# Kernel optimization log

Measured on AMD Instinct MI355X. Metric: run time of the kernel, lower is better.

Reference implementation:

```python
import jax, jax.numpy as jnp
import numpy as np

B, N, X_DIM, Y_DIM, H_DIM, R_DIM = 64, 512, 128, 128, 4096, 1024


def setup_inputs() -> dict:
    key = jax.random.key(0)
    ks = jax.random.split(key, 10)
    x = jax.random.normal(ks[0], (B, N, X_DIM), dtype=jnp.float32)
    y = jax.random.normal(ks[1], (B, N, Y_DIM), dtype=jnp.float32)
    # per-sample context lengths in [1, N]; prefix mask guarantees >=1 True per row
    lengths = jax.random.randint(ks[2], (B,), 1, N + 1)
    mask = (jnp.arange(N)[None, :] < lengths[:, None])  # [B, N] bool
    d_in = X_DIM + Y_DIM
    s1 = 1.0 / np.sqrt(d_in)
    s2 = 1.0 / np.sqrt(H_DIM)
    W1 = jax.random.uniform(ks[3], (d_in, H_DIM), jnp.float32, -s1, s1)
    b1 = jax.random.uniform(ks[4], (H_DIM,), jnp.float32, -s1, s1)
    W2 = jax.random.uniform(ks[5], (H_DIM, H_DIM), jnp.float32, -s2, s2)
    b2 = jax.random.uniform(ks[6], (H_DIM,), jnp.float32, -s2, s2)
    W3 = jax.random.uniform(ks[7], (H_DIM, R_DIM), jnp.float32, -s2, s2)
    b3 = jax.random.uniform(ks[8], (R_DIM,), jnp.float32, -s2, s2)
    return {"x": x, "y": y, "mask": mask,
            "W1": W1, "b1": b1, "W2": W2, "b2": b2, "W3": W3, "b3": b3}


def reference(x, y, mask, W1, b1, W2, b2, W3, b3):
    # Dense equivalent of gather -> MLP -> scatter_mean by batch id:
    # the MLP is pointwise over tokens, so applying it densely and taking a
    # masked mean over the point dim gives identical math to the ragged path.
    nn_in = jnp.concatenate([x, y], axis=-1)          # [B, N, x+y]
    h = jax.nn.relu(jnp.einsum('bnd,dh->bnh', nn_in, W1) + b1)
    h = jax.nn.relu(jnp.einsum('bnh,hk->bnk', h, W2) + b2)
    r = jnp.einsum('bnk,kr->bnr', h, W3) + b3          # [B, N, r_dim]
    m = mask.astype(r.dtype)[..., None]                # [B, N, 1]
    counts = jnp.maximum(m.sum(axis=1), 1.0)           # [B, 1]
    r_aggr = (r * m).sum(axis=1) / counts              # [B, r_dim]
    return r_aggr
```

## Files before the change

### kernel.cpp

```cpp
#include <hip/hip_runtime.h>


using u16 = unsigned short;
using u8 = unsigned char;
typedef float f32x4 __attribute__((ext_vector_type(4)));
typedef short s16x8 __attribute__((ext_vector_type(8)));
typedef int i32x4 __attribute__((ext_vector_type(4)));

__device__ __forceinline__ u16 f2bf(float f) {
  union { float f; unsigned u; } v; v.f = f;
  unsigned r = (v.u + 0x7fffu + ((v.u >> 16) & 1u)) >> 16;
  return (u16)r;
}


__global__ void count_k(const int* __restrict__ mask, int* __restrict__ lens) {
  int b = blockIdx.x, l = threadIdx.x;
  const int4* row = (const int4*)(mask + (size_t)b * 512);
  int4 v0 = row[l];
  int4 v1 = row[l + 64];
  int s = v0.x + v0.y + v0.z + v0.w + v1.x + v1.y + v1.z + v1.w;
  #pragma unroll
  for (int o = 32; o; o >>= 1) s += __shfl_down(s, o);
  if (l == 0) lens[b] = s;
}

__global__ void meta_k(const int* __restrict__ lens, int* __restrict__ meta) {
  if (threadIdx.x == 0) {
    int acc = 0; meta[0] = 0;
    for (int b = 0; b < 64; ++b) { acc += lens[b]; meta[b + 1] = acc; }
    meta[65] = acc;
    meta[66] = (acc + 127) >> 7;
  }
}

__global__ void tok2b_k(const int* __restrict__ meta, int* __restrict__ tok2b) {
  int i = blockIdx.x * 256 + threadIdx.x;
  int total = meta[65];
  int b = 64;
  if (i < total) {
    int lo = 0, hi = 64;
    while (hi - lo > 1) { int mid = (lo + hi) >> 1; if (meta[mid] <= i) lo = mid; else hi = mid; }
    b = lo;
  }
  tok2b[i] = b;
}

__global__ void build_a(const float* __restrict__ x, const float* __restrict__ y,
                        const int* __restrict__ meta, const int* __restrict__ tok2b,
                        u16* __restrict__ A) {
  int i4 = blockIdx.x * 256 + threadIdx.x;
  int e = i4 * 4;
  int m = e >> 8, c = e & 255;
  int total = meta[65];
  ushort4 o = {0, 0, 0, 0};
  if (m < total) {
    int b = tok2b[m], t = m - meta[b];
    const float* src = (c < 128) ? x + ((size_t)b * 512 + t) * 128 + c
                                 : y + ((size_t)b * 512 + t) * 128 + (c - 128);
    float4 v = *(const float4*)src;
    o.x = f2bf(v.x); o.y = f2bf(v.y); o.z = f2bf(v.z); o.w = f2bf(v.w);
  }
  *(ushort4*)&A[e] = o;
}

__global__ void pack_k(const float* __restrict__ W, u16* __restrict__ P,
                       int N, int NKB) {
  long c = (long)blockIdx.x * 256 + threadIdx.x;
  int lane = c & 63; long r = c >> 6;
  int s = r & 1; int j = (r >> 1) & 3; int wn = (r >> 3) & 1;
  long q = r >> 4;
  int ktb = (int)(q % NKB), nt = (int)(q / NKB);
  int k = ktb * 64 + s * 32 + (lane >> 4) * 8;
  int n = nt * 128 + wn * 64 + j * 16 + (lane & 15);
  ushort o[8];
  #pragma unroll
  for (int e = 0; e < 8; ++e) o[e] = f2bf(W[(size_t)(k + e) * N + n]);
  *(uint4*)&P[c * 8] = *(uint4*)o;
}

__global__ void colmax_k(const float* __restrict__ W, float* __restrict__ cmax) {
  int n = blockIdx.x * 256 + threadIdx.x;
  int k0 = blockIdx.y * 128;
  float m = 0.f;
  for (int k = k0; k < k0 + 128; ++k)
    m = fmaxf(m, fabsf(W[(size_t)k * 4096 + n]));
  atomicMax((int*)&cmax[n], __float_as_int(m));
}

__global__ void pack8_k(const float* __restrict__ W, const float* __restrict__ cmax,
                        char* __restrict__ P) {
  long c = (long)blockIdx.x * 256 + threadIdx.x;
  int lane = c & 63; long r = c >> 6;
  int j = r & 3; int wn = (r >> 2) & 1; long q = r >> 3;
  int ktb = (int)(q & 63), nt = (int)(q >> 6);
  int k = ktb * 64 + (lane >> 4) * 16;
  int n = nt * 128 + wn * 64 + j * 16 + (lane & 15);
  float rw = 127.0f / fmaxf(cmax[n], 1e-20f);
  char o[16];
  #pragma unroll
  for (int e = 0; e < 16; ++e) {
    int v = __float2int_rn(W[(size_t)(k + e) * 4096 + n] * rw);
    v = v > 127 ? 127 : (v < -127 ? -127 : v);
    o[e] = (char)v;
  }
  *(uint4*)&P[c * 16] = *(const uint4*)o;
}

__global__ void sn_k(const float* __restrict__ S, const int* __restrict__ lens,
                     u16* __restrict__ Sn) {
  int i4 = blockIdx.x * 256 + threadIdx.x;
  int e = i4 * 4;
  int m = e >> 12;
  float inv = (m < 64) ? (1.0f / (float)lens[m]) : 0.0f;
  float4 v = *(const float4*)(S + e);
  ushort4 o;
  o.x = f2bf(v.x * inv); o.y = f2bf(v.y * inv);
  o.z = f2bf(v.z * inv); o.w = f2bf(v.w * inv);
  *(ushort4*)&Sn[e] = o;
}

template <int MODE>
__global__ __launch_bounds__(256, 3) void gemm_k(
    const void* __restrict__ Av, int lda, const void* __restrict__ BPv,
    const float* __restrict__ bias, const float* __restrict__ cmax,
    u8* __restrict__ Hout, float* __restrict__ Sout, float* __restrict__ Fout,
    const int* __restrict__ meta, const int* __restrict__ tok2b,
    int K, int Nld, int tile0, int tile_cap) {
  constexpr bool A8 = (MODE == 1);
  constexpr int BK = A8 ? 128 : 64;
  __shared__ union {
    u16 a16[2][128 * 64];
    u8  a8[3][128 * 128];
    u8  outT8[128 * 128];
  } sm;

  const int tid = threadIdx.x;
  const int wave = tid >> 6;
  const int lane = tid & 63;
  const int wm = wave >> 1, wn = wave & 1;
  const int quad = lane >> 4, l15 = lane & 15;
  const int NKB = K >> 6;

  int nslots;
  if constexpr (MODE < 2) {
    int tc = meta[66] - tile0;
    tc = tc < 0 ? 0 : (tc > tile_cap ? tile_cap : tc);
    nslots = tc * 32;
  } else {
    nslots = gridDim.x;
  }

  for (int slot = blockIdx.x; slot < nslots; slot += gridDim.x) {
    int mt, n0, k0, kend;
    if constexpr (MODE < 2) {
      mt = slot >> 5; n0 = (slot & 31) << 7; k0 = 0; kend = K;
    } else {
      mt = 0; n0 = slot << 7; k0 = blockIdx.y * 512; kend = k0 + 512;
    }

    f32x4 accf[4][4];
    i32x4 acci[4][4];
    #pragma unroll
    for (int i = 0; i < 4; i++)
      #pragma unroll
      for (int j = 0; j < 4; j++) {
        if constexpr (A8) acci[i][j] = (i32x4){0, 0, 0, 0};
        else accf[i][j] = (f32x4){0.f, 0.f, 0.f, 0.f};
      }

    const u8* ag8[4];
    const u16* ag16[4];
    if constexpr (A8) {
      #pragma unroll
      for (int il = 0; il < 4; ++il) {
        int ci = (wave * 4 + il) * 64 + lane;
        int m = ci >> 3, c = (ci & 7) ^ (m & 7);
        ag8[il] = (const u8*)Av + (size_t)(mt * 128 + m) * lda + c * 16;
      }
    } else {
      #pragma unroll
      for (int il = 0; il < 4; ++il) {
        int ci = (wave * 4 + il) * 64 + lane;
        int m = ci >> 3, c = (ci & 7) ^ (m & 7);
        ag16[il] = (const u16*)Av + (size_t)(mt * 128 + m) * lda + c * 8;
      }
    }
    const u16* bw = nullptr;
    const u8* bw8 = nullptr;
    if constexpr (A8)
      bw8 = (const u8*)BPv + (size_t)(n0 >> 7) * NKB * 8192 + wn * 4096 + lane * 16;
    else
      bw = (const u16*)BPv + (size_t)(n0 >> 7) * NKB * 8192 + wn * 4096 + lane * 8;

    s16x8 breg0[8], breg1[8];
    i32x4 breg8_0[8], breg8_1[8];

    auto stageA = [&](int kt, int buf) {
      if constexpr (A8) {
        #pragma unroll
        for (int il = 0; il < 4; ++il)
          __builtin_amdgcn_global_load_lds(
              (const __attribute__((address_space(1))) void*)(ag8[il] + kt),
              (__attribute__((address_space(3))) void*)(&sm.a8[buf][(wave * 4 + il) * 1024]),
              16, 0, 0);
      } else {
        #pragma unroll
        for (int il = 0; il < 4; ++il)
          __builtin_amdgcn_global_load_lds(
              (const __attribute__((address_space(1))) void*)(ag16[il] + kt),
              (__attribute__((address_space(3))) void*)(&sm.a16[buf][(wave * 4 + il) * 512]),
              16, 0, 0);
      }
    };
    auto loadB = [&](int kt, int which) {
      if constexpr (A8) {
        i32x4* dst = which ? breg8_1 : breg8_0;
        const u8* p = bw8 + (size_t)(kt >> 6) * 8192;
        #pragma unroll
        for (int s = 0; s < 2; s++)
          #pragma unroll
          for (int j = 0; j < 4; j++)
            dst[s * 4 + j] = *(const i32x4*)(p + s * 8192 + j * 1024);
      } else {
        s16x8* dst = which ? breg1 : breg0;
        const u16* p = bw + (size_t)(kt >> 6) * 8192;
        #pragma unroll
        for (int j = 0; j < 4; j++)
          #pragma unroll
          for (int s = 0; s < 2; s++)
            dst[j * 2 + s] = *(const s16x8*)(p + j * 1024 + s * 512);
      }
    };
    auto compute = [&](int buf, int which) {
      if constexpr (A8) {
        const i32x4* br = which ? breg8_1 : breg8_0;
        const u8* ab = &sm.a8[0][0] + buf * 16384;
        #pragma unroll
        for (int s = 0; s < 2; ++s) {
          #pragma unroll
          for (int i = 0; i < 4; i++) {
            int m = wm * 64 + i * 16 + l15;
            int c = (s * 4 + quad) ^ (m & 7);
            i32x4 a = *(const i32x4*)&ab[(m * 8 + c) * 16];
            #pragma unroll
            for (int j = 0; j < 4; j++)
              acci[i][j] = __builtin_amdgcn_mfma_i32_16x16x64_i8(
                  a, br[s * 4 + j], acci[i][j], 0, 0, 0);
          }
        }
      } else {
        const s16x8* br = which ? breg1 : breg0;
        #pragma unroll
        for (int s = 0; s < 2; ++s) {
          s16x8 af[4];
          #pragma unroll
          for (int i = 0; i < 4; i++) {
            int m = wm * 64 + i * 16 + l15;
            int c = (s * 4 + quad) ^ (m & 7);
            af[i] = *(const s16x8*)&sm.a16[buf][(m * 8 + c) * 8];
          }
          #pragma unroll
          for (int i = 0; i < 4; i++)
            #pragma unroll
            for (int j = 0; j < 4; j++)
              accf[i][j] = __builtin_amdgcn_mfma_f32_16x16x32_bf16(
                  af[i], br[j * 2 + s], accf[i][j], 0, 0, 0);
        }
      }
    };

    if constexpr (A8) {
      stageA(k0, 0);
      stageA(k0 + BK, 1);
      loadB(k0, 0);
      const int NP = (kend - k0) / BK;
      int bufc = 0, bufs = 2;
      for (int t = 0; t < NP; t += 2) {
        int kt = k0 + t * BK;
        __builtin_amdgcn_s_waitcnt(0x0F7C);
        __builtin_amdgcn_s_barrier();
        if (t + 2 < NP) stageA(kt + 2 * BK, bufs);
        __builtin_amdgcn_sched_barrier(0);
        loadB(kt + BK, 1);
        compute(bufc, 0);
        bufc = bufc == 2 ? 0 : bufc + 1;
        bufs = bufs == 2 ? 0 : bufs + 1;
        __builtin_amdgcn_s_waitcnt(0x0F7C);
        __builtin_amdgcn_s_barrier();
        if (t + 3 < NP) stageA(kt + 3 * BK, bufs);
        __builtin_amdgcn_sched_barrier(0);
        if (t + 2 < NP) loadB(kt + 2 * BK, 0);
        compute(bufc, 1);
        bufc = bufc == 2 ? 0 : bufc + 1;
        bufs = bufs == 2 ? 0 : bufs + 1;
      }
    } else {
      stageA(k0, 0);
      loadB(k0, 0);
      const int NP = (kend - k0) / BK;
      for (int t = 0; t < NP; t += 2) {
        int kt = k0 + t * BK;
        __builtin_amdgcn_s_waitcnt(0x0F78);
        __builtin_amdgcn_s_barrier();
        stageA(kt + BK, 1);
        __builtin_amdgcn_sched_barrier(0);
        loadB(kt + BK, 1);
        compute(0, 0);
        __builtin_amdgcn_s_waitcnt(0x0F78);
        __builtin_amdgcn_s_barrier();
        if (t + 2 < NP) {
          stageA(kt + 2 * BK, 0);
          __builtin_amdgcn_sched_barrier(0);
          loadB(kt + 2 * BK, 0);
        }
        compute(1, 1);
      }
    }
    __syncthreads();

    if constexpr (MODE == 0) {
      float bb[4];
      #pragma unroll
      for (int j = 0; j < 4; j++) bb[j] = bias[n0 + wn * 64 + j * 16 + l15];
      #pragma unroll
      for (int i = 0; i < 4; i++)
        #pragma unroll
        for (int j = 0; j < 4; j++) {
          int col = wn * 64 + j * 16 + l15;
          #pragma unroll
          for (int r = 0; r < 4; r++) {
            int row = wm * 64 + i * 16 + quad * 4 + r;
            float v = accf[i][j][r] + bb[j];
            v = v > 0.f ? v : 0.f;
            int qv = (int)(v * 32.0f + 0.5f);
            if (qv > 127) qv = 127;
            sm.outT8[row * 128 + col] = (u8)qv;
          }
        }
      __syncthreads();
      #pragma unroll
      for (int u = 0; u < 4; ++u) {
        int e = u * 256 + tid;
        int row = e >> 3, c16 = (e & 7) * 16;
        *(uint4*)&Hout[(size_t)(mt * 128 + row) * Nld + n0 + c16] =
            *(const uint4*)&sm.outT8[row * 128 + c16];
      }
      __syncthreads();
    } else if constexpr (MODE == 1) {
      float bb[4], sc[4];
      #pragma unroll
      for (int j = 0; j < 4; j++) {
        int col_ = n0 + wn * 64 + j * 16 + l15;
        bb[j] = bias[col_];
        sc[j] = cmax[col_] * (1.0f / (127.0f * 32.0f));
      }
      int tb[16];
      const int gbase = tile0 * 128 + mt * 128 + wm * 64 + quad * 4;
      #pragma unroll
      for (int i = 0; i < 4; i++)
        #pragma unroll
        for (int r = 0; r < 4; r++) tb[i * 4 + r] = tok2b[gbase + i * 16 + r];
      #pragma unroll
      for (int j = 0; j < 4; j++) {
        int col = n0 + wn * 64 + j * 16 + l15;
        float sum = 0.f;
        int cb = tb[0];
        #pragma unroll
        for (int idx = 0; idx < 16; ++idx) {
          float t = (float)acci[idx >> 2][j][idx & 3] * sc[j] + bb[j];
          t = t > 0.f ? t : 0.f;
          int b = tb[idx];
          if (b != cb) {
            atomicAdd(&Sout[(size_t)cb * 4096 + col], sum);
            sum = 0.f; cb = b;
          }
          sum += t;
        }
        atomicAdd(&Sout[(size_t)cb * 4096 + col], sum);
      }
    } else {
      float bb[4];
      #pragma unroll
      for (int j = 0; j < 4; j++)
        bb[j] = (blockIdx.y == 0) ? bias[n0 + wn * 64 + j * 16 + l15] : 0.f;
      #pragma unroll
      for (int i = 0; i < 4; i++)
        #pragma unroll
        for (int j = 0; j < 4; j++) {
          int col = wn * 64 + j * 16 + l15;
          #pragma unroll
          for (int r = 0; r < 4; r++) {
            int row = wm * 64 + i * 16 + quad * 4 + r;
            if (row < 64)
              atomicAdd(&Fout[(size_t)row * Nld + n0 + col], accf[i][j][r] + bb[j]);
          }
        }
    }
  }
}

extern "C" void kernel_launch(void* const* d_in, const int* in_sizes, int n_in,
                              void* d_out, int out_size, void* d_ws, size_t ws_size,
                              hipStream_t stream) {
  const float* x  = (const float*)d_in[0];
  const float* y  = (const float*)d_in[1];
  const int* mask = (const int*)d_in[2];
  const float* W1 = (const float*)d_in[3];
  const float* b1 = (const float*)d_in[4];
  const float* W2 = (const float*)d_in[5];
  const float* b2 = (const float*)d_in[6];
  const float* W3 = (const float*)d_in[7];
  const float* b3 = (const float*)d_in[8];
  float* out = (float*)d_out;

  char* ws = (char*)d_ws;
  size_t off = 0;
  auto alloc = [&](size_t bytes) {
    char* p = ws + off;
    off += (bytes + 255) & ~(size_t)255;
    return p;
  };
  int* lens  = (int*)alloc(64 * 4);
  int* meta  = (int*)alloc(70 * 4);
  int* tok2b = (int*)alloc((size_t)32768 * 4);
  float* S   = (float*)alloc((size_t)128 * 4096 * 4);
  u16* Sn    = (u16*)alloc((size_t)128 * 4096 * 2);
  float* cm  = (float*)alloc((size_t)4096 * 4);
  u16* W1P   = (u16*)alloc((size_t)256 * 4096 * 2);
  char* W2P8 = (char*)alloc((size_t)4096 * 4096);
  u16* W3P   = (u16*)alloc((size_t)4096 * 1024 * 2);
  u16* Abuf  = (u16*)alloc((size_t)32768 * 256 * 2);
  size_t fixed = off;
  size_t h1_full = (size_t)32768 * 4096;
  int nchunks, tile_cap;
  if (ws_size >= fixed + h1_full) { nchunks = 1; tile_cap = 256; }
  else if (ws_size >= fixed + h1_full / 2) { nchunks = 2; tile_cap = 128; }
  else if (ws_size >= fixed + h1_full / 4) { nchunks = 4; tile_cap = 64; }
  else return;
  u8* H1 = (u8*)alloc(h1_full / nchunks);

  hipMemsetAsync(S, 0, (size_t)128 * 4096 * 4, stream);
  hipMemsetAsync(cm, 0, (size_t)4096 * 4, stream);
  hipMemsetAsync(out, 0, (size_t)out_size * 4, stream);
  count_k<<<64, 64, 0, stream>>>(mask, lens);
  meta_k<<<1, 64, 0, stream>>>(lens, meta);
  tok2b_k<<<128, 256, 0, stream>>>(meta, tok2b);
  build_a<<<8192, 256, 0, stream>>>(x, y, meta, tok2b, Abuf);
  pack_k<<<512, 256, 0, stream>>>(W1, W1P, 4096, 4);
  colmax_k<<<dim3(16, 32), 256, 0, stream>>>(W2, cm);
  pack8_k<<<4096, 256, 0, stream>>>(W2, cm, W2P8);
  pack_k<<<2048, 256, 0, stream>>>(W3, W3P, 1024, 64);

  for (int c = 0; c < nchunks; ++c) {
    gemm_k<0><<<dim3(768), 256, 0, stream>>>(
        Abuf + (size_t)c * tile_cap * 128 * 256, 256, W1P, b1, nullptr, H1,
        nullptr, nullptr, meta, tok2b, 256, 4096, c * tile_cap, tile_cap);
    gemm_k<1><<<dim3(768), 256, 0, stream>>>(
        H1, 4096, W2P8, b2, cm, nullptr, S, nullptr,
        meta, tok2b, 4096, 4096, c * tile_cap, tile_cap);
  }
  sn_k<<<512, 256, 0, stream>>>(S, lens, Sn);
  gemm_k<2><<<dim3(8, 8), 256, 0, stream>>>(
      Sn, 4096, W3P, b3, nullptr, nullptr, nullptr, out,
      meta, tok2b, 4096, 1024, 0, 0);
}
```

Measured before the change: 670.2 us.

## Switch int8 GEMM A-staging from triple to double buffering

Cuts the int8 A tile LDS ring from three buffers to two and restructures the K loop into fixed two-buffer phases with extra barriers between compute and restage. This lowers the LDS footprint of the union, which could allow more resident blocks. In exchange, prefetch distance shrinks and more barriers sit on the critical path, so less copy latency is hidden.

```diff
diff --git a/kernel.cpp b/kernel.cpp
--- a/kernel.cpp
+++ b/kernel.cpp
@@ -131,7 +131,7 @@
   constexpr int BK = A8 ? 128 : 64;
   __shared__ union {
     u16 a16[2][128 * 64];
-    u8  a8[3][128 * 128];
+    u8  a8[2][128 * 128];
     u8  outT8[128 * 128];
   } sm;
 
@@ -235,14 +235,13 @@
     auto compute = [&](int buf, int which) {
       if constexpr (A8) {
         const i32x4* br = which ? breg8_1 : breg8_0;
-        const u8* ab = &sm.a8[0][0] + buf * 16384;
         #pragma unroll
         for (int s = 0; s < 2; ++s) {
           #pragma unroll
           for (int i = 0; i < 4; i++) {
             int m = wm * 64 + i * 16 + l15;
             int c = (s * 4 + quad) ^ (m & 7);
-            i32x4 a = *(const i32x4*)&ab[(m * 8 + c) * 16];
+            i32x4 a = *(const i32x4*)&sm.a8[buf][(m * 8 + c) * 16];
             #pragma unroll
             for (int j = 0; j < 4; j++)
               acci[i][j] = __builtin_amdgcn_mfma_i32_16x16x64_i8(
@@ -271,29 +270,27 @@
     };
 
     if constexpr (A8) {
+      constexpr int KSTEP = 2 * BK;
       stageA(k0, 0);
-      stageA(k0 + BK, 1);
+      if (k0 + BK < kend) stageA(k0 + BK, 1);
       loadB(k0, 0);
-      const int NP = (kend - k0) / BK;
-      int bufc = 0, bufs = 2;
-      for (int t = 0; t < NP; t += 2) {
-        int kt = k0 + t * BK;
+      for (int kt = k0; kt < kend; kt += KSTEP) {
+        loadB(kt + BK, 1);
         __builtin_amdgcn_s_waitcnt(0x0F7C);
         __builtin_amdgcn_s_barrier();
-        if (t + 2 < NP) stageA(kt + 2 * BK, bufs);
-        __builtin_amdgcn_sched_barrier(0);
-        loadB(kt + BK, 1);
-        compute(bufc, 0);
-        bufc = bufc == 2 ? 0 : bufc + 1;
-        bufs = bufs == 2 ? 0 : bufs + 1;
-        __builtin_amdgcn_s_waitcnt(0x0F7C);
-        __builtin_amdgcn_s_barrier();
-        if (t + 3 < NP) stageA(kt + 3 * BK, bufs);
-        __builtin_amdgcn_sched_barrier(0);
-        if (t + 2 < NP) loadB(kt + 2 * BK, 0);
-        compute(bufc, 1);
-        bufc = bufc == 2 ? 0 : bufc + 1;
-        bufs = bufs == 2 ? 0 : bufs + 1;
+        compute(0, 0);
+        __builtin_amdgcn_s_barrier();
+        if (kt + KSTEP < kend) stageA(kt + KSTEP, 0);
+        if (kt + KSTEP < kend) {
+          loadB(kt + KSTEP, 0);
+          __builtin_amdgcn_s_waitcnt(0x0F7C);
+        } else {
+          __builtin_amdgcn_s_waitcnt(0x0F70);
+        }
+        __builtin_amdgcn_s_barrier();
+        compute(1, 1);
+        __builtin_amdgcn_s_barrier();
+        if (kt + KSTEP + BK < kend) stageA(kt + KSTEP + BK, 1);
       }
     } else {
       stageA(k0, 0);
```

Result: faster. 576.7 us (-14.0%).
